# Optimization experiments

Measured on AMD Instinct MI355X. Metric: run time of the kernel, lower is better.

## Reference

```python
import jax, jax.numpy as jnp
import numpy as np

N = 100000
D = 128
E = 1600000


def setup_inputs() -> dict:
    key = jax.random.key(0)
    k1, k2, k3, k4 = jax.random.split(key, 4)
    x = jax.random.normal(k1, (N, D), dtype=jnp.float32)
    edge_index = jax.random.randint(k2, (2, E), 0, N, dtype=jnp.int64)
    edge_weight = jax.random.uniform(k3, (E,), dtype=jnp.float32)
    x0 = jax.random.normal(k4, (N, D), dtype=jnp.float32)
    return {
        "t": jnp.zeros((), dtype=jnp.float32),
        "x": x,
        "edge_index": edge_index,
        "edge_weight": edge_weight,
        "x0": x0,
        "alpha_train": jnp.zeros((), dtype=jnp.float32),
        "beta_train": jnp.zeros((), dtype=jnp.float32),
        "source_train": jnp.zeros((), dtype=jnp.float32),
    }


def reference(t, x, edge_index, edge_weight, x0, alpha_train, beta_train, source_train):
    # sigmoid-gated diffusion/reaction coefficients
    alpha = jax.nn.sigmoid(alpha_train) * 0.1
    beta = jax.nn.sigmoid(beta_train) * 0.1
    # sparse A @ x: out[row] += w * x[col]  (torch_sparse.spmm convention)
    row, col = edge_index[0], edge_index[1]
    msgs = x[col] * edge_weight[:, None]            # [E, D]
    ax = jax.ops.segment_sum(msgs, row, num_segments=N)  # [N, D]
    diffusion = ax - x
    reaction = -(x - 1.0) * x
    f = alpha * diffusion + beta * reaction
    source_term = jnp.clip(source_train * x0, -1.0, 1.0)
    return f + source_term * 0.1
```

## Files before the change

kernel.cpp:

```cpp
#include <hip/hip_runtime.h>
#include <math.h>


#define D_FEAT 128
#define RPB 128
#define NB_MAX 800
#define SORT_CAP 2560
#define EPB 8192
#define MAXBLK 256

__device__ __forceinline__ float sigmoid_f(float v) {
    return 1.0f / (1.0f + __expf(-v));
}

__device__ __forceinline__ unsigned bf16rn(float f) {
    unsigned u = __float_as_uint(f);
    return (u + 0x7FFFu + ((u >> 16) & 1u)) >> 16;
}

__global__ __launch_bounds__(256) void cvt_kernel(const float* __restrict__ x,
                                                  unsigned short* __restrict__ xb,
                                                  int n8, int* __restrict__ cursors) {
    int i = blockIdx.x * 256 + threadIdx.x;
    if (blockIdx.x == 0 && threadIdx.x == 0) { cursors[0] = 0; cursors[1] = 0; }
    if (!xb || i >= n8) return;
    const float4* x4 = (const float4*)x;
    float4 f0 = x4[(size_t)i * 2];
    float4 f1 = x4[(size_t)i * 2 + 1];
    uint4 o;
    o.x = bf16rn(f0.x) | (bf16rn(f0.y) << 16);
    o.y = bf16rn(f0.z) | (bf16rn(f0.w) << 16);
    o.z = bf16rn(f1.x) | (bf16rn(f1.y) << 16);
    o.w = bf16rn(f1.z) | (bf16rn(f1.w) << 16);
    ((uint4*)xb)[i] = o;
}

__global__ __launch_bounds__(256) void place_kernel(const int* __restrict__ rows,
                                                    const int* __restrict__ cols,
                                                    const float* __restrict__ w,
                                                    const float* __restrict__ alpha_p,
                                                    int* __restrict__ arenaCur,
                                                    int2* __restrict__ arena,
                                                    unsigned* __restrict__ dir,
                                                    int* __restrict__ blkBase,
                                                    int E, int NB) {
    __shared__ int hist[NB_MAX];
    __shared__ int lexcl[NB_MAX];
    __shared__ int scanb[256];
    __shared__ int gbase_sh;
    int t = threadIdx.x;
    int blk = blockIdx.x;
    int base = blk * EPB;
    for (int i = t; i < NB; i += 256) hist[i] = 0;
    __syncthreads();

    int rr[32];
#pragma unroll
    for (int k = 0; k < 32; ++k) {
        int e = base + k * 256 + t;
        rr[k] = (e < E) ? rows[e] : -1;
    }
#pragma unroll
    for (int k = 0; k < 32; ++k)
        if (rr[k] >= 0) atomicAdd(&hist[rr[k] >> 7], 1);
    __syncthreads();

    const int CHK = 4;
    int loc[CHK];
    int run = 0;
#pragma unroll
    for (int k = 0; k < CHK; ++k) {
        int idx = t * CHK + k;
        int v = (idx < NB) ? hist[idx] : 0;
        loc[k] = run; run += v;
    }
    scanb[t] = run;
    __syncthreads();
    for (int d = 1; d < 256; d <<= 1) {
        int tv = (t >= d) ? scanb[t - d] : 0;
        __syncthreads();
        scanb[t] += tv;
        __syncthreads();
    }
    int excl = scanb[t] - run;
    int total = scanb[255];
#pragma unroll
    for (int k = 0; k < CHK; ++k) {
        int idx = t * CHK + k;
        if (idx < NB) lexcl[idx] = excl + loc[k];
    }
    if (t == 0) gbase_sh = atomicAdd(arenaCur, total);
    __syncthreads();
    for (int i = t; i < NB; i += 256) hist[i] = lexcl[i];
    __syncthreads();
    int gbase = gbase_sh;
    const float alpha = sigmoid_f(alpha_p[0]) * 0.1f;

#pragma unroll
    for (int g = 0; g < 4; ++g) {
        int   cc[8];
        float wwv[8];
#pragma unroll
        for (int k = 0; k < 8; ++k) {
            int e = base + (g * 8 + k) * 256 + t;
            cc[k]  = (e < E) ? cols[e] : 0;
            wwv[k] = (e < E) ? w[e]    : 0.0f;
        }
#pragma unroll
        for (int k = 0; k < 8; ++k) {
            int r = rr[g * 8 + k];
            if (r < 0) continue;
            int bkt = r >> 7;
            int pos = atomicAdd(&hist[bkt], 1);
            arena[gbase + pos] = make_int2(((r & 127) << 17) | cc[k],
                                           __float_as_int(wwv[k] * alpha));
        }
    }
    __syncthreads();

    for (int b = t; b < NB; b += 256) {
        int le  = lexcl[b];
        int len = ((b + 1 < NB) ? lexcl[b + 1] : total) - le;
        dir[(size_t)blk * NB + b] = ((unsigned)le << 14) | (unsigned)len;
    }
    if (t == 0) blkBase[blk] = gbase;
}

__global__ __launch_bounds__(256) void sort_kernel(const int2* __restrict__ arena,
                                                   const unsigned* __restrict__ dir,
                                                   const int* __restrict__ blkBase,
                                                   int nBlk,
                                                   unsigned* __restrict__ col_w,
                                                   int* __restrict__ outCur,
                                                   int* __restrict__ off,
                                                   int* __restrict__ bstart2,
                                                   int N, int NB) {
    __shared__ int2 sbuf[SORT_CAP];
    __shared__ unsigned obuf[SORT_CAP];
    __shared__ int pre[MAXBLK + 1];
    __shared__ int abase[MAXBLK];
    __shared__ int scanb[256];
    __shared__ int hist[RPB];
    __shared__ int hscan[RPB];
    __shared__ int cursor[RPB];
    __shared__ int gb_sh;
    int b = blockIdx.x;
    int t = threadIdx.x;

    int len = 0;
    if (t < nBlk) {
        unsigned d = dir[(size_t)t * NB + b];
        len = (int)(d & 0x3FFFu);
        abase[t] = blkBase[t] + (int)(d >> 14);
    }
    scanb[t] = len;
    __syncthreads();
    for (int d = 1; d < 256; d <<= 1) {
        int tv = (t >= d) ? scanb[t - d] : 0;
        __syncthreads();
        scanb[t] += tv;
        __syncthreads();
    }
    if (t < nBlk) pre[t] = scanb[t] - len;
    if (t == 0) {
        int total = scanb[nBlk - 1];
        pre[nBlk] = total;
        gb_sh = atomicAdd(outCur, total);
    }
    if (t < RPB) hist[t] = 0;
    __syncthreads();
    int cntb  = pre[nBlk];
    int gbase = gb_sh;
    bool fast = (cntb <= SORT_CAP);

    for (int i = t; i < cntb; i += 256) {
        int lo = 0, hi = nBlk;
        while (hi - lo > 1) { int m = (lo + hi) >> 1; if (pre[m] <= i) lo = m; else hi = m; }
        int2 rec = arena[abase[lo] + (i - pre[lo])];
        if (fast) sbuf[i] = rec;
        atomicAdd(&hist[rec.x >> 17], 1);
    }
    __syncthreads();

    int v = 0;
    if (t < RPB) { v = hist[t]; hscan[t] = v; }
    __syncthreads();
    for (int d = 1; d < RPB; d <<= 1) {
        int tv = (t >= d && t < RPB) ? hscan[t - d] : 0;
        __syncthreads();
        if (t < RPB) hscan[t] += tv;
        __syncthreads();
    }
    if (t < RPB) {
        int incl = hscan[t];
        int excl = incl - v;
        int row = b * RPB + t;
        if (row < N) off[row] = gbase + incl;
        cursor[t] = fast ? excl : (gbase + excl);
    }
    if (t == 0) bstart2[b] = gbase;
    __syncthreads();

    if (fast) {
        for (int i = t; i < cntb; i += 256) {
            int2 r = sbuf[i];
            int rl = r.x >> 17;
            int pos = atomicAdd(&cursor[rl], 1);
            unsigned wb = bf16rn(__int_as_float(r.y)) & 0x7FFFu;
            obuf[pos] = (wb << 17) | (unsigned)(r.x & 0x1FFFF);
        }
        __syncthreads();
        for (int i = t; i < cntb; i += 256)
            col_w[gbase + i] = obuf[i];
    } else {
        for (int i = t; i < cntb; i += 256) {
            int lo = 0, hi = nBlk;
            while (hi - lo > 1) { int m = (lo + hi) >> 1; if (pre[m] <= i) lo = m; else hi = m; }
            int2 r = arena[abase[lo] + (i - pre[lo])];
            int rl = r.x >> 17;
            int pos = atomicAdd(&cursor[rl], 1);
            unsigned wb = bf16rn(__int_as_float(r.y)) & 0x7FFFu;
            col_w[pos] = (wb << 17) | (unsigned)(r.x & 0x1FFFF);
        }
    }
}

__global__ void gather_bf16_kernel(const float* __restrict__ x,
                                   const unsigned short* __restrict__ xb,
                                   const float* __restrict__ x0,
                                   const int* __restrict__ off,
                                   const int* __restrict__ bstart2,
                                   const unsigned* __restrict__ col_w,
                                   const float* __restrict__ alpha_p,
                                   const float* __restrict__ beta_p,
                                   const float* __restrict__ src_p,
                                   float* __restrict__ out, int N) {
    const float alpha = sigmoid_f(alpha_p[0]) * 0.1f;
    const float beta  = sigmoid_f(beta_p[0]) * 0.1f;
    const float src   = src_p[0];

    int gtid = blockIdx.x * blockDim.x + threadIdx.x;
    int row  = gtid >> 6;
    if (row >= N) return;
    int lane  = threadIdx.x & 63;
    int half  = lane >> 5;
    int flane = lane & 31;

    int start = ((row & 127) == 0) ? bstart2[row >> 7] : off[row - 1];
    int end   = off[row];

    const uint2* xb2 = (const uint2*)xb;
    float4 a0 = make_float4(0.f, 0.f, 0.f, 0.f);
    float4 a1 = make_float4(0.f, 0.f, 0.f, 0.f);
    float4 a2 = make_float4(0.f, 0.f, 0.f, 0.f);
    float4 a3 = make_float4(0.f, 0.f, 0.f, 0.f);

#define BF16_FMA(ACC, V, W)                                                    \
    {                                                                          \
        float b0 = __uint_as_float((V).x << 16);                               \
        float b1 = __uint_as_float((V).x & 0xFFFF0000u);                       \
        float b2 = __uint_as_float((V).y << 16);                               \
        float b3 = __uint_as_float((V).y & 0xFFFF0000u);                       \
        ACC.x += (W) * b0; ACC.y += (W) * b1;                                  \
        ACC.z += (W) * b2; ACC.w += (W) * b3;                                  \
    }
#define UNPACK_W(P) __uint_as_float(((P) >> 17) << 16)

    int j = start + half;
    for (; j + 6 < end; j += 8) {
        unsigned p0 = col_w[j];
        unsigned p1 = col_w[j + 2];
        unsigned p2 = col_w[j + 4];
        unsigned p3 = col_w[j + 6];
        uint2 v0 = xb2[(size_t)(p0 & 0x1FFFF) * 32 + flane];
        uint2 v1 = xb2[(size_t)(p1 & 0x1FFFF) * 32 + flane];
        uint2 v2 = xb2[(size_t)(p2 & 0x1FFFF) * 32 + flane];
        uint2 v3 = xb2[(size_t)(p3 & 0x1FFFF) * 32 + flane];
        float w0 = UNPACK_W(p0);
        float w1 = UNPACK_W(p1);
        float w2 = UNPACK_W(p2);
        float w3 = UNPACK_W(p3);
        BF16_FMA(a0, v0, w0);
        BF16_FMA(a1, v1, w1);
        BF16_FMA(a2, v2, w2);
        BF16_FMA(a3, v3, w3);
    }
    for (; j + 2 < end; j += 4) {
        unsigned p0 = col_w[j];
        unsigned p1 = col_w[j + 2];
        uint2 v0 = xb2[(size_t)(p0 & 0x1FFFF) * 32 + flane];
        uint2 v1 = xb2[(size_t)(p1 & 0x1FFFF) * 32 + flane];
        float w0 = UNPACK_W(p0);
        float w1 = UNPACK_W(p1);
        BF16_FMA(a0, v0, w0);
        BF16_FMA(a1, v1, w1);
    }
    if (j < end) {
        unsigned p = col_w[j];
        uint2 v = xb2[(size_t)(p & 0x1FFFF) * 32 + flane];
        float wv = UNPACK_W(p);
        BF16_FMA(a0, v, wv);
    }
#undef BF16_FMA
#undef UNPACK_W

    float4 acc;
    acc.x = (a0.x + a1.x) + (a2.x + a3.x);
    acc.y = (a0.y + a1.y) + (a2.y + a3.y);
    acc.z = (a0.z + a1.z) + (a2.z + a3.z);
    acc.w = (a0.w + a1.w) + (a2.w + a3.w);

    acc.x += __shfl_xor(acc.x, 32);
    acc.y += __shfl_xor(acc.y, 32);
    acc.z += __shfl_xor(acc.z, 32);
    acc.w += __shfl_xor(acc.w, 32);

    if (half == 0) {
        long long base = (long long)row * 32 + flane;
        float4 xv = ((const float4*)x)[base];
        float4 x0v = make_float4(0.f, 0.f, 0.f, 0.f);
        if (src != 0.0f)
            x0v = ((const float4*)x0)[base];
        float xs[4]  = {xv.x, xv.y, xv.z, xv.w};
        float zs[4]  = {x0v.x, x0v.y, x0v.z, x0v.w};
        float as[4]  = {acc.x, acc.y, acc.z, acc.w};
        float os[4];
#pragma unroll
        for (int k = 0; k < 4; ++k) {
            float reaction = -(xs[k] - 1.0f) * xs[k];
            float st = fminf(fmaxf(src * zs[k], -1.0f), 1.0f);
            os[k] = as[k] - alpha * xs[k] + beta * reaction + st * 0.1f;
        }
        ((float4*)out)[base] = make_float4(os[0], os[1], os[2], os[3]);
    }
}

__global__ void gather_f32_kernel(const float* __restrict__ x,
                                  const float* __restrict__ x0,
                                  const int* __restrict__ off,
                                  const int* __restrict__ bstart2,
                                  const unsigned* __restrict__ col_w,
                                  const float* __restrict__ alpha_p,
                                  const float* __restrict__ beta_p,
                                  const float* __restrict__ src_p,
                                  float* __restrict__ out, int N) {
    const float alpha = sigmoid_f(alpha_p[0]) * 0.1f;
    const float beta  = sigmoid_f(beta_p[0]) * 0.1f;
    const float src   = src_p[0];

    int gtid = blockIdx.x * blockDim.x + threadIdx.x;
    int row  = gtid >> 6;
    if (row >= N) return;
    int lane  = threadIdx.x & 63;
    int half  = lane >> 5;
    int flane = lane & 31;

    int start = ((row & 127) == 0) ? bstart2[row >> 7] : off[row - 1];
    int end   = off[row];

    const float4* x4 = (const float4*)x;
    float4 a0 = make_float4(0.f, 0.f, 0.f, 0.f);
    float4 a1 = make_float4(0.f, 0.f, 0.f, 0.f);

    int j = start + half;
    for (; j + 2 < end; j += 4) {
        unsigned p0 = col_w[j];
        unsigned p1 = col_w[j + 2];
        float4 v0 = x4[(long long)(p0 & 0x1FFFF) * 32 + flane];
        float4 v1 = x4[(long long)(p1 & 0x1FFFF) * 32 + flane];
        float w0 = __uint_as_float((p0 >> 17) << 16);
        float w1 = __uint_as_float((p1 >> 17) << 16);
        a0.x += w0 * v0.x; a0.y += w0 * v0.y; a0.z += w0 * v0.z; a0.w += w0 * v0.w;
        a1.x += w1 * v1.x; a1.y += w1 * v1.y; a1.z += w1 * v1.z; a1.w += w1 * v1.w;
    }
    if (j < end) {
        unsigned p = col_w[j];
        float4 v = x4[(long long)(p & 0x1FFFF) * 32 + flane];
        float wv = __uint_as_float((p >> 17) << 16);
        a0.x += wv * v.x; a0.y += wv * v.y; a0.z += wv * v.z; a0.w += wv * v.w;
    }
    float4 acc;
    acc.x = a0.x + a1.x; acc.y = a0.y + a1.y;
    acc.z = a0.z + a1.z; acc.w = a0.w + a1.w;

    acc.x += __shfl_xor(acc.x, 32);
    acc.y += __shfl_xor(acc.y, 32);
    acc.z += __shfl_xor(acc.z, 32);
    acc.w += __shfl_xor(acc.w, 32);

    if (half == 0) {
        long long base = (long long)row * 32 + flane;
        float4 xv  = x4[base];
        float4 x0v = make_float4(0.f, 0.f, 0.f, 0.f);
        if (src != 0.0f)
            x0v = ((const float4*)x0)[base];
        float xs[4]  = {xv.x, xv.y, xv.z, xv.w};
        float zs[4]  = {x0v.x, x0v.y, x0v.z, x0v.w};
        float as[4]  = {acc.x, acc.y, acc.z, acc.w};
        float os[4];
#pragma unroll
        for (int k = 0; k < 4; ++k) {
            float reaction = -(xs[k] - 1.0f) * xs[k];
            float st = fminf(fmaxf(src * zs[k], -1.0f), 1.0f);
            os[k] = as[k] - alpha * xs[k] + beta * reaction + st * 0.1f;
        }
        ((float4*)out)[base] = make_float4(os[0], os[1], os[2], os[3]);
    }
}

extern "C" void kernel_launch(void* const* d_in, const int* in_sizes, int n_in,
                              void* d_out, int out_size, void* d_ws, size_t ws_size,
                              hipStream_t stream) {
    const float* x   = (const float*)d_in[1];
    const int*   ei  = (const int*)d_in[2];
    const float* ew  = (const float*)d_in[3];
    const float* x0  = (const float*)d_in[4];
    const float* alp = (const float*)d_in[5];
    const float* bet = (const float*)d_in[6];
    const float* src = (const float*)d_in[7];
    float* out = (float*)d_out;

    const int E = in_sizes[3];
    const int N = out_size / D_FEAT;
    const int* rows = ei;
    const int* cols = ei + E;

    const int NB   = (N + RPB - 1) / RPB;
    const int nBlk = (E + EPB - 1) / EPB;

    char* ws = (char*)d_ws;
    char* ws_end = (char*)d_ws + ws_size;
    int*      off     = (int*)ws;      ws += ((size_t)N * 4 + 15) & ~15ull;
    int*      bstart2 = (int*)ws;      ws += ((size_t)NB * 4 + 15) & ~15ull;
    unsigned* col_w   = (unsigned*)ws; ws += ((size_t)E * 4 + 15) & ~15ull;

    char* ob = (char*)d_out;
    int2*     arena   = (int2*)ob;       ob += ((size_t)E * 8 + 15) & ~15ull;
    unsigned* dir     = (unsigned*)ob;   ob += ((size_t)nBlk * NB * 4 + 15) & ~15ull;
    int*      blkBase = (int*)ob;        ob += ((size_t)nBlk * 4 + 15) & ~15ull;
    int*      cursors = (int*)ob;        ob += 16;
    if (ob > (char*)d_out + out_size) {
        arena   = (int2*)ws;     ws += ((size_t)E * 8 + 15) & ~15ull;
        dir     = (unsigned*)ws; ws += ((size_t)nBlk * NB * 4 + 15) & ~15ull;
        blkBase = (int*)ws;      ws += ((size_t)nBlk * 4 + 15) & ~15ull;
        cursors = (int*)ws;      ws += 16;
    }

    unsigned short* xb = nullptr;
    size_t xb_bytes = ((size_t)N * D_FEAT * 2 + 15) & ~15ull;
    if (ws + xb_bytes <= ws_end) {
        xb = (unsigned short*)ws;  ws += xb_bytes;
    }

    {
        int n8 = (N * D_FEAT) / 8;
        int grid = xb ? (n8 + 255) / 256 : 1;
        cvt_kernel<<<grid, 256, 0, stream>>>(x, xb, n8, cursors);
    }
    place_kernel<<<nBlk, 256, 0, stream>>>(rows, cols, ew, alp,
                                           &cursors[0], arena, dir, blkBase, E, NB);
    sort_kernel<<<NB, 256, 0, stream>>>(arena, dir, blkBase, nBlk,
                                        col_w, &cursors[1], off, bstart2, N, NB);
    {
        long long threads = (long long)N * 64;
        int grid = (int)((threads + 255) / 256);
        if (xb)
            gather_bf16_kernel<<<grid, 256, 0, stream>>>(x, xb, x0, off, bstart2,
                                                         col_w, alp, bet, src, out, N);
        else
            gather_f32_kernel<<<grid, 256, 0, stream>>>(x, x0, off, bstart2,
                                                        col_w, alp, bet, src, out, N);
    }
}
```

Before: 283.6 us.

## Shrink placement blocks and walk arena segments per source block in sort

Edges per placement block drop from 8192 to 2048, so about 782 blocks run instead of 196, which should help occupancy in the placement pass. The directory is transposed to bucket-major order so each sort block reads a contiguous row, and the length and offset bit fields are narrowed to match. The sort kernel now gives each thread whole per-block segments to walk, replacing the per-element binary search over prefix sums. The risk is that per-thread segment loops are short and uneven, and that uncoalesced arena reads plus the 800-entry shared arrays may offset the gain.

```diff
diff --git a/kernel.cpp b/kernel.cpp
--- a/kernel.cpp
+++ b/kernel.cpp
@@ -6,8 +6,9 @@
 #define RPB 128
 #define NB_MAX 800
 #define SORT_CAP 2560
-#define EPB 8192
-#define MAXBLK 256
+#define EPB 2048
+#define EPT 8
+#define NBLK_MAX 800
 
 __device__ __forceinline__ float sigmoid_f(float v) {
     return 1.0f / (1.0f + __expf(-v));
@@ -43,7 +44,7 @@
                                                     int2* __restrict__ arena,
                                                     unsigned* __restrict__ dir,
                                                     int* __restrict__ blkBase,
-                                                    int E, int NB) {
+                                                    int E, int NB, int nBlk) {
     __shared__ int hist[NB_MAX];
     __shared__ int lexcl[NB_MAX];
     __shared__ int scanb[256];
@@ -54,14 +55,14 @@
     for (int i = t; i < NB; i += 256) hist[i] = 0;
     __syncthreads();
 
-    int rr[32];
-#pragma unroll
-    for (int k = 0; k < 32; ++k) {
+    int rr[EPT];
+#pragma unroll
+    for (int k = 0; k < EPT; ++k) {
         int e = base + k * 256 + t;
         rr[k] = (e < E) ? rows[e] : -1;
     }
 #pragma unroll
-    for (int k = 0; k < 32; ++k)
+    for (int k = 0; k < EPT; ++k)
         if (rr[k] >= 0) atomicAdd(&hist[rr[k] >> 7], 1);
     __syncthreads();
 
@@ -96,32 +97,29 @@
     int gbase = gbase_sh;
     const float alpha = sigmoid_f(alpha_p[0]) * 0.1f;
 
-#pragma unroll
-    for (int g = 0; g < 4; ++g) {
-        int   cc[8];
-        float wwv[8];
-#pragma unroll
-        for (int k = 0; k < 8; ++k) {
-            int e = base + (g * 8 + k) * 256 + t;
-            cc[k]  = (e < E) ? cols[e] : 0;
-            wwv[k] = (e < E) ? w[e]    : 0.0f;
-        }
-#pragma unroll
-        for (int k = 0; k < 8; ++k) {
-            int r = rr[g * 8 + k];
-            if (r < 0) continue;
-            int bkt = r >> 7;
-            int pos = atomicAdd(&hist[bkt], 1);
-            arena[gbase + pos] = make_int2(((r & 127) << 17) | cc[k],
-                                           __float_as_int(wwv[k] * alpha));
-        }
+    int   cc[EPT];
+    float wwv[EPT];
+#pragma unroll
+    for (int k = 0; k < EPT; ++k) {
+        int e = base + k * 256 + t;
+        cc[k]  = (e < E) ? cols[e] : 0;
+        wwv[k] = (e < E) ? w[e]    : 0.0f;
+    }
+#pragma unroll
+    for (int k = 0; k < EPT; ++k) {
+        int r = rr[k];
+        if (r < 0) continue;
+        int bkt = r >> 7;
+        int pos = atomicAdd(&hist[bkt], 1);
+        arena[gbase + pos] = make_int2(((r & 127) << 17) | cc[k],
+                                       __float_as_int(wwv[k] * alpha));
     }
     __syncthreads();
 
     for (int b = t; b < NB; b += 256) {
         int le  = lexcl[b];
         int len = ((b + 1 < NB) ? lexcl[b + 1] : total) - le;
-        dir[(size_t)blk * NB + b] = ((unsigned)le << 14) | (unsigned)len;
+        dir[(size_t)b * nBlk + blk] = ((unsigned)le << 12) | (unsigned)len;
     }
     if (t == 0) blkBase[blk] = gbase;
 }
@@ -137,8 +135,8 @@
                                                    int N, int NB) {
     __shared__ int2 sbuf[SORT_CAP];
     __shared__ unsigned obuf[SORT_CAP];
-    __shared__ int pre[MAXBLK + 1];
-    __shared__ int abase[MAXBLK];
+    __shared__ int pre[NBLK_MAX + 1];
+    __shared__ int abase[NBLK_MAX];
     __shared__ int scanb[256];
     __shared__ int hist[RPB];
     __shared__ int hscan[RPB];
@@ -147,13 +145,21 @@
     int b = blockIdx.x;
     int t = threadIdx.x;
 
-    int len = 0;
-    if (t < nBlk) {
-        unsigned d = dir[(size_t)t * NB + b];
-        len = (int)(d & 0x3FFFu);
-        abase[t] = blkBase[t] + (int)(d >> 14);
-    }
-    scanb[t] = len;
+    const int CHK = 4;
+    int lloc[CHK];
+    int run = 0;
+#pragma unroll
+    for (int k = 0; k < CHK; ++k) {
+        int c = t * CHK + k;
+        int len = 0;
+        if (c < nBlk) {
+            unsigned d = dir[(size_t)b * nBlk + c];
+            len = (int)(d & 0xFFFu);
+            abase[c] = blkBase[c] + (int)(d >> 12);
+        }
+        lloc[k] = run; run += len;
+    }
+    scanb[t] = run;
     __syncthreads();
     for (int d = 1; d < 256; d <<= 1) {
         int tv = (t >= d) ? scanb[t - d] : 0;
@@ -161,9 +167,14 @@
         scanb[t] += tv;
         __syncthreads();
     }
-    if (t < nBlk) pre[t] = scanb[t] - len;
+    int excl = scanb[t] - run;
+#pragma unroll
+    for (int k = 0; k < CHK; ++k) {
+        int c = t * CHK + k;
+        if (c < nBlk) pre[c] = excl + lloc[k];
+    }
     if (t == 0) {
-        int total = scanb[nBlk - 1];
+        int total = scanb[255];
         pre[nBlk] = total;
         gb_sh = atomicAdd(outCur, total);
     }
@@ -173,12 +184,15 @@
     int gbase = gb_sh;
     bool fast = (cntb <= SORT_CAP);
 
-    for (int i = t; i < cntb; i += 256) {
-        int lo = 0, hi = nBlk;
-        while (hi - lo > 1) { int m = (lo + hi) >> 1; if (pre[m] <= i) lo = m; else hi = m; }
-        int2 rec = arena[abase[lo] + (i - pre[lo])];
-        if (fast) sbuf[i] = rec;
-        atomicAdd(&hist[rec.x >> 17], 1);
+    for (int c = t; c < nBlk; c += 256) {
+        int p = pre[c];
+        int n = pre[c + 1] - p;
+        int a = abase[c];
+        for (int k = 0; k < n; ++k) {
+            int2 rec = arena[a + k];
+            if (fast) sbuf[p + k] = rec;
+            atomicAdd(&hist[rec.x >> 17], 1);
+        }
     }
     __syncthreads();
 
@@ -193,10 +207,10 @@
     }
     if (t < RPB) {
         int incl = hscan[t];
-        int excl = incl - v;
+        int ex2  = incl - v;
         int row = b * RPB + t;
         if (row < N) off[row] = gbase + incl;
-        cursor[t] = fast ? excl : (gbase + excl);
+        cursor[t] = fast ? ex2 : (gbase + ex2);
     }
     if (t == 0) bstart2[b] = gbase;
     __syncthreads();
@@ -213,14 +227,17 @@
         for (int i = t; i < cntb; i += 256)
             col_w[gbase + i] = obuf[i];
     } else {
-        for (int i = t; i < cntb; i += 256) {
-            int lo = 0, hi = nBlk;
-            while (hi - lo > 1) { int m = (lo + hi) >> 1; if (pre[m] <= i) lo = m; else hi = m; }
-            int2 r = arena[abase[lo] + (i - pre[lo])];
-            int rl = r.x >> 17;
-            int pos = atomicAdd(&cursor[rl], 1);
-            unsigned wb = bf16rn(__int_as_float(r.y)) & 0x7FFFu;
-            col_w[pos] = (wb << 17) | (unsigned)(r.x & 0x1FFFF);
+        for (int c = t; c < nBlk; c += 256) {
+            int p = pre[c];
+            int n = pre[c + 1] - p;
+            int a = abase[c];
+            for (int k = 0; k < n; ++k) {
+                int2 r = arena[a + k];
+                int rl = r.x >> 17;
+                int pos = atomicAdd(&cursor[rl], 1);
+                unsigned wb = bf16rn(__int_as_float(r.y)) & 0x7FFFu;
+                col_w[pos] = (wb << 17) | (unsigned)(r.x & 0x1FFFF);
+            }
         }
     }
 }
@@ -436,12 +453,12 @@
 
     char* ob = (char*)d_out;
     int2*     arena   = (int2*)ob;       ob += ((size_t)E * 8 + 15) & ~15ull;
-    unsigned* dir     = (unsigned*)ob;   ob += ((size_t)nBlk * NB * 4 + 15) & ~15ull;
+    unsigned* dir     = (unsigned*)ob;   ob += ((size_t)NB * nBlk * 4 + 15) & ~15ull;
     int*      blkBase = (int*)ob;        ob += ((size_t)nBlk * 4 + 15) & ~15ull;
     int*      cursors = (int*)ob;        ob += 16;
     if (ob > (char*)d_out + out_size) {
         arena   = (int2*)ws;     ws += ((size_t)E * 8 + 15) & ~15ull;
-        dir     = (unsigned*)ws; ws += ((size_t)nBlk * NB * 4 + 15) & ~15ull;
+        dir     = (unsigned*)ws; ws += ((size_t)NB * nBlk * 4 + 15) & ~15ull;
         blkBase = (int*)ws;      ws += ((size_t)nBlk * 4 + 15) & ~15ull;
         cursors = (int*)ws;      ws += 16;
     }
@@ -458,7 +475,8 @@
         cvt_kernel<<<grid, 256, 0, stream>>>(x, xb, n8, cursors);
     }
     place_kernel<<<nBlk, 256, 0, stream>>>(rows, cols, ew, alp,
-                                           &cursors[0], arena, dir, blkBase, E, NB);
+                                           &cursors[0], arena, dir, blkBase,
+                                           E, NB, nBlk);
     sort_kernel<<<NB, 256, 0, stream>>>(arena, dir, blkBase, nBlk,
                                         col_w, &cursors[1], off, bstart2, N, NB);
     {
```

After: 291.7 us. +2.8%, slower.
